# Optimization experiments

Hardware: AMD Instinct MI355X
Metric: run time of the kernel (lower is better)

Reference implementation:

```python
import jax, jax.numpy as jnp
import numpy as np

B, N, D, P, H = 16, 1024, 512, 512, 8
E = P // H  # head dim = 64


def layer_norm(x, g, b, eps=1e-5):
    mu = jnp.mean(x, axis=-1, keepdims=True)
    var = jnp.var(x, axis=-1, keepdims=True)
    return (x - mu) * jax.lax.rsqrt(var + eps) * g + b


def setup_inputs() -> dict:
    key = jax.random.key(0)
    ks = jax.random.split(key, 12)
    s = 0.02
    inp = {
        "x": jax.random.normal(ks[0], (B, N, D), dtype=jnp.float32),
        "Wq": jax.random.normal(ks[1], (D, P), dtype=jnp.float32) * s,
        "bq": jnp.zeros((P,), jnp.float32),
        "Wk": jax.random.normal(ks[2], (D, P), dtype=jnp.float32) * s,
        "bk": jnp.zeros((P,), jnp.float32),
        "Wv": jax.random.normal(ks[3], (D, P), dtype=jnp.float32) * s,
        "bv": jnp.zeros((P,), jnp.float32),
        "Wo": jax.random.normal(ks[4], (P, D), dtype=jnp.float32) * s,
        "bo": jnp.zeros((D,), jnp.float32),
        "ln1_g": jnp.ones((D,), jnp.float32),
        "ln1_b": jnp.zeros((D,), jnp.float32),
        "W1": jax.random.normal(ks[5], (D, 4 * D), dtype=jnp.float32) * s,
        "b1": jnp.zeros((4 * D,), jnp.float32),
        "W2": jax.random.normal(ks[6], (4 * D, D), dtype=jnp.float32) * s,
        "b2": jnp.zeros((D,), jnp.float32),
        "ln2_g": jnp.ones((D,), jnp.float32),
        "ln2_b": jnp.zeros((D,), jnp.float32),
    }
    return inp


def reference(x, Wq, bq, Wk, bk, Wv, bv, Wo, bo, ln1_g, ln1_b, W1, b1, W2, b2, ln2_g, ln2_b):
    # dropout layers are identity in eval mode
    q = (x @ Wq + bq).reshape(B, N, H, E)
    k = (x @ Wk + bk).reshape(B, N, H, E)
    v = (x @ Wv + bv).reshape(B, N, H, E)
    scale = 1.0 / jnp.sqrt(jnp.float32(E))
    scores = jnp.einsum('blhe,bshe->bhls', q, k)  # [B,H,L,S]
    A = jax.nn.softmax(scale * scores, axis=-1)
    V = jnp.einsum('bhls,bshd->blhd', A, v).reshape(B, N, P)
    att = V @ Wo + bo
    x1 = layer_norm(x + att, ln1_g, ln1_b)
    # FFN: 1x1 convs over channel dim == per-token linears, exact GELU
    ff = jax.nn.gelu(x1 @ W1 + b1, approximate=False) @ W2 + b2
    return layer_norm(x1 + ff, ln2_g, ln2_b)
```

## Files before the change

kernel.cpp:

```cpp
#include <hip/hip_runtime.h>
#include <hip/hip_bf16.h>

typedef __hip_bfloat16 bf16;
typedef __bf16 bf16x8 __attribute__((ext_vector_type(8)));
typedef __bf16 bf16x4 __attribute__((ext_vector_type(4)));
typedef float f32x4 __attribute__((ext_vector_type(4)));

static __device__ __forceinline__ f32x4 mfma16(bf16x8 a, bf16x8 b, f32x4 c) {
  return __builtin_amdgcn_mfma_f32_16x16x32_bf16(a, b, c, 0, 0, 0);
}
static __device__ __forceinline__ bf16x8 ld8(const bf16* p) {
  return *reinterpret_cast<const bf16x8*>(p);
}
static __device__ __forceinline__ float toF(float v) { return v; }
static __device__ __forceinline__ float toF(bf16 v) { return __bfloat162float(v); }
static __device__ __forceinline__ void stF(float* p, float v) { *p = v; }
static __device__ __forceinline__ void stF(bf16* p, float v) { *p = __float2bfloat16(v); }

typedef __attribute__((address_space(1))) void gvoid;
typedef __attribute__((address_space(3))) void lvoid;
static __device__ __forceinline__ void gl2lds16(const bf16* g, bf16* l) {
  __builtin_amdgcn_global_load_lds((gvoid*)g, (lvoid*)l, 16, 0, 0);
}

__global__ __launch_bounds__(256) void cvt_kernel(const float* __restrict__ in,
                                                  bf16* __restrict__ out) {
  long i = (long)blockIdx.x * 256 + threadIdx.x;
  float4 v = reinterpret_cast<const float4*>(in)[i];
  bf16x4 o;
  o[0] = __float2bfloat16(v.x); o[1] = __float2bfloat16(v.y);
  o[2] = __float2bfloat16(v.z); o[3] = __float2bfloat16(v.w);
  reinterpret_cast<bf16x4*>(out)[i] = o;
}

__global__ void prep_weights(const float* __restrict__ Wq, const float* __restrict__ Wk,
                             const float* __restrict__ Wv, const float* __restrict__ Wo,
                             const float* __restrict__ W1, const float* __restrict__ W2,
                             bf16* __restrict__ Wtqkv, bf16* __restrict__ WtO,
                             bf16* __restrict__ Wt1, bf16* __restrict__ Wt2) {
  int id = blockIdx.x;
  const float* in;
  bf16* out;
  int K, N, n0, k0;
  if (id < 1024) {
    int which = id >> 8, t = id & 255;
    K = 512; N = 512;
    n0 = (t & 15) * 32; k0 = (t >> 4) * 32;
    if (which == 0)      { in = Wq; out = Wtqkv; }
    else if (which == 1) { in = Wk; out = Wtqkv + (size_t)512 * 512; }
    else if (which == 2) { in = Wv; out = Wtqkv + (size_t)1024 * 512; }
    else                 { in = Wo; out = WtO; }
  } else if (id < 2048) {
    int t = id - 1024;
    in = W1; out = Wt1; K = 512; N = 2048;
    n0 = (t & 63) * 32; k0 = (t >> 6) * 32;
  } else {
    int t = id - 2048;
    in = W2; out = Wt2; K = 2048; N = 512;
    n0 = (t & 15) * 32; k0 = (t >> 4) * 32;
  }
  __shared__ float tile[32][33];
  int tx = threadIdx.x, ty = threadIdx.y;
#pragma unroll
  for (int j = 0; j < 32; j += 8)
    tile[ty + j][tx] = in[(long)(k0 + ty + j) * N + n0 + tx];
  __syncthreads();
#pragma unroll
  for (int j = 0; j < 32; j += 8)
    out[(long)(n0 + ty + j) * K + k0 + tx] = __float2bfloat16(tile[tx][ty + j]);
}

template <int MODE>
__global__ __launch_bounds__(256) void gemm_kernel(
    const bf16* __restrict__ A, const bf16* __restrict__ Wt,
    const float* __restrict__ b0, const float* __restrict__ b1_,
    const float* __restrict__ b2_, bf16* C0, bf16* C1, bf16* C2,
    int K, int ldc, int mmask, int mshift) {
  __shared__ alignas(16) bf16 As[2][128 * 32];
  __shared__ alignas(16) bf16 Bs[2][128 * 32];
  const int tid = threadIdx.x;
  const int wave = tid >> 6, lane = tid & 63;
  const int lr = lane & 15, lq = lane >> 4;
  const int L = blockIdx.x;
  const int m0 = (L & mmask) * 128, n0 = (L >> mshift) * 128;
  const int wm = (wave >> 1) * 64, wn = (wave & 1) * 64;

  const int srow0 = (wave * 2) * 16 + (lane >> 2);
  const int srow1 = (wave * 2 + 1) * 16 + (lane >> 2);
  const int scol = (lane & 3) * 8;
  const bf16* Ag0 = A + (long)(m0 + srow0) * K + scol;
  const bf16* Ag1 = A + (long)(m0 + srow1) * K + scol;
  const bf16* Bg0 = Wt + (long)(n0 + srow0) * K + scol;
  const bf16* Bg1 = Wt + (long)(n0 + srow1) * K + scol;
  const int so0 = (wave * 2) * 16 * 32;
  const int so1 = (wave * 2 + 1) * 16 * 32;

  f32x4 acc[4][4] = {};

  gl2lds16(Ag0, &As[0][so0]);
  gl2lds16(Ag1, &As[0][so1]);
  gl2lds16(Bg0, &Bs[0][so0]);
  gl2lds16(Bg1, &Bs[0][so1]);
  __syncthreads();

  int p = 0;
  for (int k0 = 0; k0 < K; k0 += 32) {
    int kn = k0 + 32;
    if (kn < K) {
      gl2lds16(Ag0 + kn, &As[p ^ 1][so0]);
      gl2lds16(Ag1 + kn, &As[p ^ 1][so1]);
      gl2lds16(Bg0 + kn, &Bs[p ^ 1][so0]);
      gl2lds16(Bg1 + kn, &Bs[p ^ 1][so1]);
    }
    bf16x8 af[4], bfr[4];
#pragma unroll
    for (int i = 0; i < 4; ++i) af[i] = ld8(&As[p][(wm + i * 16 + lr) * 32 + lq * 8]);
#pragma unroll
    for (int j = 0; j < 4; ++j) bfr[j] = ld8(&Bs[p][(wn + j * 16 + lr) * 32 + lq * 8]);
#pragma unroll
    for (int i = 0; i < 4; ++i)
#pragma unroll
      for (int j = 0; j < 4; ++j) acc[i][j] = mfma16(af[i], bfr[j], acc[i][j]);
    __syncthreads();
    p ^= 1;
  }

  const float* bias = b0;
  bf16* C = C0;
  int cb = n0;
  bool vmode = false;
  if (MODE == 2) {
    if (n0 >= 1024)     { bias = b2_; C = C2; cb = n0 - 1024; vmode = true; }
    else if (n0 >= 512) { bias = b1_; C = C1; cb = n0 - 512; }
  }

#pragma unroll
  for (int i = 0; i < 4; ++i) {
#pragma unroll
    for (int j = 0; j < 4; ++j) {
      int col = cb + wn + j * 16 + lr;
      float bv = bias[col];
#pragma unroll
      for (int rr = 0; rr < 4; ++rr) {
        int row = m0 + wm + i * 16 + lq * 4 + rr;
        float v = acc[i][j][rr] + bv;
        if (MODE == 1) v = 0.5f * v * (1.0f + erff(v * 0.70710678118654752f));
        if (MODE == 2 && vmode) {
          int hh = col >> 6, e = col & 63;
          int bb = row >> 10, tok = row & 1023;
          C[(((long)((bb * 8 + hh) * 64 + e)) << 10) + tok] = __float2bfloat16(v);
        } else {
          C[(long)row * ldc + col] = __float2bfloat16(v);
        }
      }
    }
  }
}

__global__ __launch_bounds__(256) void attn_splitk(
    const bf16* __restrict__ Q, const bf16* __restrict__ Km,
    const bf16* __restrict__ Vt, bf16* __restrict__ Op,
    float* __restrict__ lsum) {
  constexpr int SP = 72;
  __shared__ alignas(16) bf16 Pall[4][64 * SP];
  __shared__ alignas(16) bf16 Ks[2][2][64][32];
  __shared__ alignas(16) bf16 Vs[2][2][64][32];
  const int tid = threadIdx.x;
  const int wave = tid >> 6, lane = tid & 63;
  const int lr = lane & 15, lq = lane >> 4;
  const int L = blockIdx.x;
  const int bh = ((L >> 6) << 3) | (L & 7);
  const int qh = (L >> 3) & 7;
  const int qc = qh & 3, half = qh >> 2;
  const int h = bh & 7, b = bh >> 3;
  const int q0 = qc * 256 + wave * 64;
  bf16* P = Pall[wave];
  const float Cc = 0.18033688011112042f;

  bf16x8 qf[4][2];
#pragma unroll
  for (int qs = 0; qs < 4; ++qs) {
    const bf16* qrow = Q + (long)(b * 1024 + q0 + qs * 16 + lr) * 512 + h * 64;
    qf[qs][0] = ld8(qrow + lq * 8);
    qf[qs][1] = ld8(qrow + 32 + lq * 8);
  }
  const bf16* kbase = Km + (long)(b * 1024 + half * 512) * 512 + h * 64;
  const bf16* vbase = Vt + (long)((b * 8 + h) * 64) * 1024 + half * 512;

  const int sr = wave * 16 + (lane >> 2);
  const int sc = (lane & 3) * 8;
  const bf16* Kg = kbase + (long)sr * 512 + sc;
  const bf16* Vg = vbase + (long)sr * 1024 + sc;

  auto stage = [&](int kb, int p) {
#pragma unroll
    for (int kk = 0; kk < 2; ++kk)
      gl2lds16(Kg + (long)kb * 64 * 512 + kk * 32, &Ks[p][kk][wave * 16][0]);
#pragma unroll
    for (int kk = 0; kk < 2; ++kk)
      gl2lds16(Vg + kb * 64 + kk * 32, &Vs[p][kk][wave * 16][0]);
  };

  bf16x8 ones;
#pragma unroll
  for (int k = 0; k < 8; ++k) ones[k] = __float2bfloat16(1.0f);

  f32x4 oacc[4][4] = {};
  f32x4 lacc[4] = {};

  stage(0, 0);
  __syncthreads();

  int p = 0;
  for (int kb = 0; kb < 8; ++kb) {
    if (kb < 7) stage(kb + 1, p ^ 1);
#pragma unroll
    for (int kt = 0; kt < 4; ++kt) {
      bf16x8 kf0 = ld8(&Ks[p][0][kt * 16 + lr][lq * 8]);
      bf16x8 kf1 = ld8(&Ks[p][1][kt * 16 + lr][lq * 8]);
#pragma unroll
      for (int qs = 0; qs < 4; ++qs) {
        f32x4 t = {};
        t = mfma16(kf0, qf[qs][0], t);
        t = mfma16(kf1, qf[qs][1], t);
        bf16x4 pk;
#pragma unroll
        for (int rr = 0; rr < 4; ++rr) pk[rr] = __float2bfloat16(exp2f(t[rr] * Cc));
        *reinterpret_cast<bf16x4*>(&P[(qs * 16 + lr) * SP + kt * 16 + lq * 4]) = pk;
      }
    }
    __builtin_amdgcn_sched_barrier(0);
    bf16x8 pf[4][2];
#pragma unroll
    for (int qs = 0; qs < 4; ++qs) {
      pf[qs][0] = ld8(&P[(qs * 16 + lr) * SP + lq * 8]);
      pf[qs][1] = ld8(&P[(qs * 16 + lr) * SP + 32 + lq * 8]);
    }
#pragma unroll
    for (int qs = 0; qs < 4; ++qs) {
      lacc[qs] = mfma16(pf[qs][0], ones, lacc[qs]);
      lacc[qs] = mfma16(pf[qs][1], ones, lacc[qs]);
    }
#pragma unroll
    for (int j0 = 0; j0 < 4; ++j0) {
      bf16x8 vf0 = ld8(&Vs[p][0][j0 * 16 + lr][lq * 8]);
      bf16x8 vf1 = ld8(&Vs[p][1][j0 * 16 + lr][lq * 8]);
#pragma unroll
      for (int qs = 0; qs < 4; ++qs) {
        oacc[qs][j0] = mfma16(pf[qs][0], vf0, oacc[qs][j0]);
        oacc[qs][j0] = mfma16(pf[qs][1], vf1, oacc[qs][j0]);
      }
    }
    __builtin_amdgcn_sched_barrier(0);
    __syncthreads();
    p ^= 1;
  }

  bf16* Oh = Op + (size_t)half * ((size_t)16384 * 512);
#pragma unroll
  for (int qs = 0; qs < 4; ++qs)
#pragma unroll
    for (int rr = 0; rr < 4; ++rr)
#pragma unroll
      for (int j0 = 0; j0 < 4; ++j0)
        Oh[(long)(b * 1024 + q0 + qs * 16 + lq * 4 + rr) * 512 + h * 64 + j0 * 16 + lr] =
            __float2bfloat16(oacc[qs][j0][rr]);
  if (lr == 0) {
    float* lp = lsum + (size_t)half * 131072 + ((size_t)(b * 8 + h) << 10);
#pragma unroll
    for (int qs = 0; qs < 4; ++qs)
#pragma unroll
      for (int rr = 0; rr < 4; ++rr)
        lp[q0 + qs * 16 + lq * 4 + rr] = lacc[qs][rr];
  }
}

__global__ __launch_bounds__(256) void attn_combine(
    const bf16* __restrict__ Op, const float* __restrict__ lsum,
    bf16* __restrict__ O) {
  long i = (long)blockIdx.x * 256 + threadIdx.x;
  long idx = i * 8;
  int tok = (int)(idx >> 9), col = (int)(idx & 511);
  int b = tok >> 10, q = tok & 1023, h = col >> 6;
  int li = (b * 8 + h) * 1024 + q;
  float inv = 1.0f / (lsum[li] + lsum[131072 + li]);
  bf16x8 a = ld8(Op + idx);
  bf16x8 c = ld8(Op + (size_t)16384 * 512 + idx);
  bf16x8 o;
#pragma unroll
  for (int k = 0; k < 8; ++k)
    o[k] = __float2bfloat16(((float)a[k] + (float)c[k]) * inv);
  *reinterpret_cast<bf16x8*>(O + idx) = o;
}

__global__ __launch_bounds__(256) void attn_kernel(
    const bf16* Q, const bf16* __restrict__ Km,
    const bf16* __restrict__ Vt, bf16* O) {
  constexpr int SP = 72;
  __shared__ alignas(16) bf16 Pall[4][64 * SP];
  const int tid = threadIdx.x;
  const int wave = tid >> 6, lane = tid & 63;
  const int lr = lane & 15, lq = lane >> 4;
  const int L = blockIdx.x;
  const int bh = ((L >> 5) << 3) | (L & 7);
  const int qc = (L >> 3) & 3;
  const int h = bh & 7, b = bh >> 3;
  const int q0 = qc * 256 + wave * 64;
  bf16* P = Pall[wave];
  const float Cc = 0.18033688011112042f;

  bf16x8 qf[4][2];
#pragma unroll
  for (int qs = 0; qs < 4; ++qs) {
    const bf16* qrow = Q + (long)(b * 1024 + q0 + qs * 16 + lr) * 512 + h * 64;
    qf[qs][0] = ld8(qrow + lq * 8);
    qf[qs][1] = ld8(qrow + 32 + lq * 8);
  }
  const bf16* kbase = Km + (long)(b * 1024) * 512 + h * 64;
  const bf16* vbase = Vt + (long)((b * 8 + h) * 64) * 1024;

  bf16x8 ones;
#pragma unroll
  for (int k = 0; k < 8; ++k) ones[k] = __float2bfloat16(1.0f);

  f32x4 oacc[4][4] = {};
  f32x4 lacc[4] = {};

  for (int kb = 0; kb < 16; ++kb) {
#pragma unroll
    for (int kt = 0; kt < 4; ++kt) {
      const bf16* krow = kbase + (long)(kb * 64 + kt * 16 + lr) * 512;
      bf16x8 kf0 = ld8(krow + lq * 8);
      bf16x8 kf1 = ld8(krow + 32 + lq * 8);
#pragma unroll
      for (int qs = 0; qs < 4; ++qs) {
        f32x4 t = {};
        t = mfma16(kf0, qf[qs][0], t);
        t = mfma16(kf1, qf[qs][1], t);
        bf16x4 pk;
#pragma unroll
        for (int rr = 0; rr < 4; ++rr) pk[rr] = __float2bfloat16(exp2f(t[rr] * Cc));
        *reinterpret_cast<bf16x4*>(&P[(qs * 16 + lr) * SP + kt * 16 + lq * 4]) = pk;
      }
    }
    __builtin_amdgcn_sched_barrier(0);
    bf16x8 pf[4][2];
#pragma unroll
    for (int qs = 0; qs < 4; ++qs) {
      pf[qs][0] = ld8(&P[(qs * 16 + lr) * SP + lq * 8]);
      pf[qs][1] = ld8(&P[(qs * 16 + lr) * SP + 32 + lq * 8]);
    }
#pragma unroll
    for (int qs = 0; qs < 4; ++qs) {
      lacc[qs] = mfma16(pf[qs][0], ones, lacc[qs]);
      lacc[qs] = mfma16(pf[qs][1], ones, lacc[qs]);
    }
#pragma unroll
    for (int j0 = 0; j0 < 4; ++j0) {
      const bf16* vrow = vbase + (long)(j0 * 16 + lr) * 1024 + kb * 64;
      bf16x8 vf0 = ld8(vrow + lq * 8);
      bf16x8 vf1 = ld8(vrow + 32 + lq * 8);
#pragma unroll
      for (int qs = 0; qs < 4; ++qs) {
        oacc[qs][j0] = mfma16(pf[qs][0], vf0, oacc[qs][j0]);
        oacc[qs][j0] = mfma16(pf[qs][1], vf1, oacc[qs][j0]);
      }
    }
    __builtin_amdgcn_sched_barrier(0);
  }

#pragma unroll
  for (int qs = 0; qs < 4; ++qs)
#pragma unroll
    for (int rr = 0; rr < 4; ++rr) {
      float lv = 1.0f / lacc[qs][rr];
#pragma unroll
      for (int j0 = 0; j0 < 4; ++j0)
        O[(long)(b * 1024 + q0 + qs * 16 + lq * 4 + rr) * 512 + h * 64 + j0 * 16 + lr] =
            __float2bfloat16(oacc[qs][j0][rr] * lv);
    }
}

template <typename TX, typename TO>
__global__ __launch_bounds__(256) void add_ln_kernel(
    const TX* __restrict__ X, const bf16* __restrict__ Y,
    const float* __restrict__ g, const float* __restrict__ bb,
    TO* __restrict__ out) {
  const int row = blockIdx.x, t = threadIdx.x;
  __shared__ float s1[4], s2[4];
  long base = (long)row * 512;
  float v0 = toF(X[base + t]) + toF(Y[base + t]);
  float v1 = toF(X[base + 256 + t]) + toF(Y[base + 256 + t]);
  float s = v0 + v1, q = v0 * v0 + v1 * v1;
#pragma unroll
  for (int o = 32; o > 0; o >>= 1) {
    s += __shfl_down(s, o);
    q += __shfl_down(q, o);
  }
  int wv = t >> 6;
  if ((t & 63) == 0) { s1[wv] = s; s2[wv] = q; }
  __syncthreads();
  float St = s1[0] + s1[1] + s1[2] + s1[3];
  float Qt = s2[0] + s2[1] + s2[2] + s2[3];
  float mean = St * (1.f / 512.f);
  float var = Qt * (1.f / 512.f) - mean * mean;
  float rs = rsqrtf(var + 1e-5f);
  stF(&out[base + t], (v0 - mean) * rs * g[t] + bb[t]);
  stF(&out[base + 256 + t], (v1 - mean) * rs * g[256 + t] + bb[256 + t]);
}

extern "C" void kernel_launch(void* const* d_in, const int* in_sizes, int n_in,
                              void* d_out, int out_size, void* d_ws, size_t ws_size,
                              hipStream_t stream) {
  const float* x    = (const float*)d_in[0];
  const float* Wq   = (const float*)d_in[1];
  const float* bq   = (const float*)d_in[2];
  const float* Wk   = (const float*)d_in[3];
  const float* bk   = (const float*)d_in[4];
  const float* Wv   = (const float*)d_in[5];
  const float* bv   = (const float*)d_in[6];
  const float* Wo   = (const float*)d_in[7];
  const float* bo   = (const float*)d_in[8];
  const float* ln1g = (const float*)d_in[9];
  const float* ln1b = (const float*)d_in[10];
  const float* W1   = (const float*)d_in[11];
  const float* b1   = (const float*)d_in[12];
  const float* W2   = (const float*)d_in[13];
  const float* b2   = (const float*)d_in[14];
  const float* ln2g = (const float*)d_in[15];
  const float* ln2b = (const float*)d_in[16];
  float* out = (float*)d_out;

  char* ws = (char*)d_ws;
  size_t off = 0;
  auto alloc = [&](size_t bytes) {
    char* p = ws + off;
    off += (bytes + 255) & ~(size_t)255;
    return (bf16*)p;
  };
  bf16* Wtqkv = alloc((size_t)1536 * 512 * 2);
  bf16* WtO   = alloc((size_t)512 * 512 * 2);
  bf16* Wt1   = alloc((size_t)512 * 2048 * 2);
  bf16* Wt2   = alloc((size_t)2048 * 512 * 2);
  const size_t SB = (size_t)16384 * 512 * 2;

  dim3 tb(32, 8);

  if (ws_size >= (size_t)104 * 1024 * 1024) {
    bf16* xb  = alloc(SB);
    bf16* kb  = alloc(SB);
    bf16* qb  = alloc(SB);
    bf16* vtb = alloc(SB);
    bf16* p0  = alloc(SB);
    bf16* p1  = alloc(SB);
    float* lsum = (float*)alloc((size_t)2 * 131072 * 4);
    bf16* ff1 = qb;
    bf16* ff2 = xb;
    (void)p1;

    cvt_kernel<<<8192, 256, 0, stream>>>(x, xb);
    prep_weights<<<3072, tb, 0, stream>>>(Wq, Wk, Wv, Wo, W1, W2,
                                          Wtqkv, WtO, Wt1, Wt2);
    gemm_kernel<2><<<1536, 256, 0, stream>>>(xb, Wtqkv, bq, bk, bv,
                                             qb, kb, vtb, 512, 512, 127, 7);
    attn_splitk<<<1024, 256, 0, stream>>>(qb, kb, vtb, p0, lsum);
    attn_combine<<<4096, 256, 0, stream>>>(p0, lsum, qb);
    gemm_kernel<0><<<512, 256, 0, stream>>>(qb, WtO, bo, nullptr, nullptr,
                                            vtb, nullptr, nullptr, 512, 512, 127, 7);
    add_ln_kernel<bf16, bf16><<<16384, 256, 0, stream>>>(xb, vtb, ln1g, ln1b, kb);
    gemm_kernel<1><<<2048, 256, 0, stream>>>(kb, Wt1, b1, nullptr, nullptr,
                                             ff1, nullptr, nullptr, 512, 2048, 127, 7);
    gemm_kernel<0><<<512, 256, 0, stream>>>(ff1, Wt2, b2, nullptr, nullptr,
                                            ff2, nullptr, nullptr, 2048, 512, 127, 7);
    add_ln_kernel<bf16, float><<<16384, 256, 0, stream>>>(kb, ff2, ln2g, ln2b, out);
  } else {
    bf16* xb  = alloc(SB);
    bf16* kb  = alloc(SB);
    bf16* qb  = alloc(SB);
    bf16* vtb = alloc(SB);
    bf16* fb  = alloc(SB / 2);
    bf16* ff1 = qb;

    cvt_kernel<<<8192, 256, 0, stream>>>(x, xb);
    prep_weights<<<3072, tb, 0, stream>>>(Wq, Wk, Wv, Wo, W1, W2,
                                          Wtqkv, WtO, Wt1, Wt2);
    gemm_kernel<2><<<1536, 256, 0, stream>>>(xb, Wtqkv, bq, bk, bv,
                                             qb, kb, vtb, 512, 512, 127, 7);
    attn_kernel<<<512, 256, 0, stream>>>(qb, kb, vtb, qb);
    gemm_kernel<0><<<512, 256, 0, stream>>>(qb, WtO, bo, nullptr, nullptr,
                                            vtb, nullptr, nullptr, 512, 512, 127, 7);
    add_ln_kernel<bf16, bf16><<<16384, 256, 0, stream>>>(xb, vtb, ln1g, ln1b, kb);

    for (int hh = 0; hh < 2; ++hh) {
      const bf16* x1h = kb + (size_t)hh * 8192 * 512;
      gemm_kernel<1><<<1024, 256, 0, stream>>>(x1h, Wt1, b1, nullptr, nullptr,
                                               ff1, nullptr, nullptr, 512, 2048, 63, 6);
      gemm_kernel<0><<<256, 256, 0, stream>>>(ff1, Wt2, b2, nullptr, nullptr,
                                              fb, nullptr, nullptr, 2048, 512, 63, 6);
      add_ln_kernel<bf16, float><<<8192, 256, 0, stream>>>(x1h, fb, ln2g, ln2b,
                                                           out + (size_t)hh * 8192 * 512);
    }
  }
}
```

Before: 401.4 us.

## Triple-buffer GEMM LDS staging with a prefetch distance of two tiles

```diff
diff --git a/kernel.cpp b/kernel.cpp
--- a/kernel.cpp
+++ b/kernel.cpp
@@ -76,8 +76,8 @@
     const float* __restrict__ b0, const float* __restrict__ b1_,
     const float* __restrict__ b2_, bf16* C0, bf16* C1, bf16* C2,
     int K, int ldc, int mmask, int mshift) {
-  __shared__ alignas(16) bf16 As[2][128 * 32];
-  __shared__ alignas(16) bf16 Bs[2][128 * 32];
+  __shared__ alignas(16) bf16 As[3][128 * 32];
+  __shared__ alignas(16) bf16 Bs[3][128 * 32];
   const int tid = threadIdx.x;
   const int wave = tid >> 6, lane = tid & 63;
   const int lr = lane & 15, lq = lane >> 4;
@@ -97,32 +97,39 @@
 
   f32x4 acc[4][4] = {};
 
-  gl2lds16(Ag0, &As[0][so0]);
-  gl2lds16(Ag1, &As[0][so1]);
-  gl2lds16(Bg0, &Bs[0][so0]);
-  gl2lds16(Bg1, &Bs[0][so1]);
-  __syncthreads();
-
-  int p = 0;
-  for (int k0 = 0; k0 < K; k0 += 32) {
-    int kn = k0 + 32;
-    if (kn < K) {
-      gl2lds16(Ag0 + kn, &As[p ^ 1][so0]);
-      gl2lds16(Ag1 + kn, &As[p ^ 1][so1]);
-      gl2lds16(Bg0 + kn, &Bs[p ^ 1][so0]);
-      gl2lds16(Bg1 + kn, &Bs[p ^ 1][so1]);
-    }
+  auto stage = [&](int k0, int buf) {
+    gl2lds16(Ag0 + k0, &As[buf][so0]);
+    gl2lds16(Ag1 + k0, &As[buf][so1]);
+    gl2lds16(Bg0 + k0, &Bs[buf][so0]);
+    gl2lds16(Bg1 + k0, &Bs[buf][so1]);
+  };
+
+  stage(0, 0);
+  stage(32, 1);
+
+  const int nk = K >> 5;
+  int cur = 0, sb = 2;
+  for (int t = 0; t < nk; ++t) {
+    if (t < nk - 1) {
+      asm volatile("s_waitcnt vmcnt(4)" ::: "memory");
+    } else {
+      asm volatile("s_waitcnt vmcnt(0)" ::: "memory");
+    }
+    __builtin_amdgcn_s_barrier();
+    if (t < nk - 2) stage((t + 2) << 5, sb);
+
     bf16x8 af[4], bfr[4];
 #pragma unroll
-    for (int i = 0; i < 4; ++i) af[i] = ld8(&As[p][(wm + i * 16 + lr) * 32 + lq * 8]);
-#pragma unroll
-    for (int j = 0; j < 4; ++j) bfr[j] = ld8(&Bs[p][(wn + j * 16 + lr) * 32 + lq * 8]);
+    for (int i = 0; i < 4; ++i) af[i] = ld8(&As[cur][(wm + i * 16 + lr) * 32 + lq * 8]);
+#pragma unroll
+    for (int j = 0; j < 4; ++j) bfr[j] = ld8(&Bs[cur][(wn + j * 16 + lr) * 32 + lq * 8]);
 #pragma unroll
     for (int i = 0; i < 4; ++i)
 #pragma unroll
       for (int j = 0; j < 4; ++j) acc[i][j] = mfma16(af[i], bfr[j], acc[i][j]);
-    __syncthreads();
-    p ^= 1;
+
+    cur = (cur == 2) ? 0 : cur + 1;
+    sb = (sb == 2) ? 0 : sb + 1;
   }
 
   const float* bias = b0;
```

After: 386.8 us. 1.04x faster.
